# Kernel optimization log

Measured on AMD Instinct MI355X. Metric: run time of the kernel, lower is better.

## Reference

```python
import jax, jax.numpy as jnp
import numpy as np

EPS = 0.01        # TopK_custom default epsilon
MAX_ITER = 200    # TopK_custom default max_iter
GAMMA_DISC = 0.99 # RMAB discount factor (python float in original forward)
BUDGET = 40       # RMABSolver budget == soft top-k k


def setup_inputs() -> dict:
    key = jax.random.key(0)
    k1, k2 = jax.random.split(key)
    B, N = 128, 2048
    T = jax.random.uniform(k1, (B, N, 2, 2, 2), dtype=jnp.float32) + 1e-3
    T = T / T.sum(-1, keepdims=True)  # valid transition probabilities
    state = jax.random.randint(k2, (B, N), 0, 2)
    return {"T": T, "state": state}


def _whittle_indices(T, g):
    # T: [B, N, 2, 2, 2] (start_state, action, end_state); returns [B, N, 2]
    ones = jnp.ones_like(T[..., 0, 0, 0])
    zeros = jnp.zeros_like(ones)
    r1 = jnp.stack([ones,  g * T[..., 0, 0, 0] - 1, g * T[..., 0, 0, 1]], -1)
    r2 = jnp.stack([zeros, g * T[..., 0, 1, 0] - 1, g * T[..., 0, 1, 1]], -1)
    r3 = jnp.stack([ones,  g * T[..., 1, 0, 0],     g * T[..., 1, 0, 1] - 1], -1)
    r4 = jnp.stack([zeros, g * T[..., 1, 1, 0],     g * T[..., 1, 1, 1] - 1], -1)
    A1_s0 = jnp.stack([r1, r2, r3], -2)
    A2_s0 = jnp.stack([r1, r2, r4], -2)
    A1_s1 = jnp.stack([r3, r4, r1], -2)
    A2_s1 = jnp.stack([r3, r4, r2], -2)
    b_s0 = jnp.array([0.0, 0.0, -1.0], dtype=T.dtype)
    b_s1 = jnp.array([-1.0, -1.0, 0.0], dtype=T.dtype)

    def solve(A, b):
        bb = jnp.broadcast_to(b, A.shape[:-1])[..., None]
        return jnp.linalg.solve(A, bb)[..., 0]

    c1_s0 = solve(A1_s0, b_s0)
    c2_s0 = solve(A2_s0, b_s0)
    c1_s1 = solve(A1_s1, b_s1)
    c2_s1 = solve(A2_s1, b_s1)

    m_s0 = (c1_s0[..., 0] + 1.0 + g * (T[..., 1, 0, 0] * c1_s0[..., 1] + T[..., 1, 0, 1] * c1_s0[..., 2])
            >= 1.0 + g * (T[..., 1, 1, 0] * c1_s0[..., 1] + T[..., 1, 1, 1] * c1_s0[..., 2]))
    m_s1 = (c1_s1[..., 0] + g * (T[..., 0, 0, 0] * c1_s1[..., 1] + T[..., 0, 0, 1] * c1_s1[..., 2])
            >= g * (T[..., 0, 1, 0] * c1_s1[..., 1] + T[..., 0, 1, 1] * c1_s1[..., 2]))
    w0 = jnp.where(m_s0, c1_s0[..., 0], c2_s0[..., 0])
    w1 = jnp.where(m_s1, c1_s1[..., 0], c2_s1[..., 0])
    return jnp.stack([w0, w1], -1)


def _soft_topk(scores, k, eps, n_iter):
    # scores: [B, N]; Sinkhorn soft top-k (Xie et al. 2020). Returns Gamma [B, N, 2].
    n = scores.shape[-1]
    s = scores[..., None]                              # [B, N, 1]
    anchors = jnp.array([0.0, 1.0], dtype=scores.dtype)
    C_raw = (s - anchors) ** 2                         # [B, N, 2]
    C = C_raw / jnp.max(C_raw, axis=(-2, -1), keepdims=True)
    eps_log_mu = eps * jnp.log(jnp.asarray(1.0 / n, dtype=scores.dtype))
    nu = jnp.array([k / n, (n - k) / n], dtype=scores.dtype)[None, :]  # [1, 2]
    eps_log_nu = eps * jnp.log(nu)
    f0 = jnp.zeros(C.shape[:-1] + (1,), C.dtype)       # [B, N, 1]
    g0 = jnp.zeros(C.shape[:-2] + (1, 2), C.dtype)     # [B, 1, 2]

    @jax.checkpoint
    def step(carry, _):
        f, g = carry
        f = -eps * jax.nn.logsumexp(-(C - g) / eps, axis=-1, keepdims=True) + eps_log_mu
        g = -eps * jax.nn.logsumexp(-(C - f) / eps, axis=-2, keepdims=True) + eps_log_nu
        return (f, g), None

    (f, g), _ = jax.lax.scan(step, (f0, g0), None, length=n_iter)
    return jnp.exp((-C + f + g) / eps)


def reference(T, state):
    W = _whittle_indices(T, GAMMA_DISC)                       # [B, N, 2]
    W_state = jnp.take_along_axis(W, state[..., None], axis=-1)[..., 0]  # [B, N]
    Gamma = _soft_topk(-W_state, BUDGET, EPS, MAX_ITER)       # [B, N, 2]
    return Gamma[..., 0] * W_state.shape[-1]                  # act: [B, N]
```

## Files before the change

kernel.cpp:

```cpp
#include <hip/hip_runtime.h>

#define N_ARMS   2048
#define NTHREADS 256
#define EPB      8
#define N_ITER   200
#define KBUDGET  40.0f

template <int CTRL>
__device__ __forceinline__ float dpp_mov0(float x) {
    return __int_as_float(__builtin_amdgcn_update_dpp(0, __float_as_int(x), CTRL, 0xf, 0xf, true));
}
__device__ __forceinline__ float wave_sum64(float x) {
    x += dpp_mov0<0x111>(x);
    x += dpp_mov0<0x112>(x);
    x += dpp_mov0<0x114>(x);
    x += dpp_mov0<0x118>(x);
    x += dpp_mov0<0x142>(x);
    x += dpp_mov0<0x143>(x);
    return __int_as_float(__builtin_amdgcn_readlane(__float_as_int(x), 63));
}
__device__ __forceinline__ float wave_max64(float x) {
    x = fmaxf(x, dpp_mov0<0x111>(x));
    x = fmaxf(x, dpp_mov0<0x112>(x));
    x = fmaxf(x, dpp_mov0<0x114>(x));
    x = fmaxf(x, dpp_mov0<0x118>(x));
    x = fmaxf(x, dpp_mov0<0x142>(x));
    x = fmaxf(x, dpp_mov0<0x143>(x));
    return __int_as_float(__builtin_amdgcn_readlane(__float_as_int(x), 63));
}

__device__ __forceinline__ void solve3(
    float a00, float a01, float a02,
    float a10, float a11, float a12,
    float a20, float a21, float a22,
    float b0, float b1, float b2,
    float& x0, float& x1, float& x2)
{
    float M00 = a11 * a22 - a12 * a21;
    float M01 = a10 * a22 - a12 * a20;
    float M02 = a10 * a21 - a11 * a20;
    float det = a00 * M00 - a01 * M01 + a02 * M02;
    float inv = 1.0f / det;
    float N0  = b1 * a22 - a12 * b2;
    float N1  = b1 * a21 - a11 * b2;
    float N2  = a10 * b2 - b1 * a20;
    x0 = (b0 * M00 - a01 * N0 + a02 * N1) * inv;
    x1 = (a00 * N0 - b0 * M01 + a02 * N2) * inv;
    x2 = (a00 * (a11 * b2 - b1 * a21) - a01 * N2 + b0 * M02) * inv;
}

__global__ __launch_bounds__(NTHREADS, 1) void rmab_kernel(
    const float* __restrict__ T, const int* __restrict__ state,
    float* __restrict__ out)
{
    const int b    = blockIdx.x;
    const int tid  = threadIdx.x;
    const int lane = tid & 63;
    const int wid  = tid >> 6;
    const float gd = 0.99f;
    const float K_T = 100.0f * 1.4426950408889634f;

    const float* Tb  = T + (size_t)b * N_ARMS * 8;
    const int*   stb = state + (size_t)b * N_ARMS;

    float c0r[EPB], c1r[EPB];
    float mt[EPB];
    float sig[EPB];
    float cmax_local = 0.0f;

    #pragma unroll
    for (int e = 0; e < EPB; ++e) {
        int i = e * NTHREADS + tid;
        const float4* p = (const float4*)(Tb + (size_t)i * 8);
        float4 T0 = p[0];
        float4 T1 = p[1];
        int st = stb[i];
        bool s1 = (st != 0);

        float r1y = gd * T0.x - 1.0f, r1z = gd * T0.y;
        float r2y = gd * T0.z - 1.0f, r2z = gd * T0.w;
        float r3y = gd * T1.x,        r3z = gd * T1.y - 1.0f;
        float r4y = gd * T1.z,        r4z = gd * T1.w - 1.0f;

        float a01 = s1 ? r3y : r1y, a02 = s1 ? r3z : r1z;
        float a11 = s1 ? r4y : r2y, a12 = s1 ? r4z : r2z;
        float c21 = s1 ? r1y : r3y, c22 = s1 ? r1z : r3z;
        float d21 = s1 ? r2y : r4y, d22 = s1 ? r2z : r4z;
        float bv0 = s1 ? -1.0f : 0.0f;
        float bv1 = s1 ? -1.0f : 0.0f;
        float bv2 = s1 ?  0.0f : -1.0f;

        float x0, x1, x2;
        solve3(1.0f, a01, a02,  0.0f, a11, a12,  1.0f, c21, c22,
               bv0, bv1, bv2, x0, x1, x2);
        float y0, y1u, y2u;
        solve3(1.0f, a01, a02,  0.0f, a11, a12,  0.0f, d21, d22,
               bv0, bv1, bv2, y0, y1u, y2u);

        float p0 = s1 ? T0.x : T1.x;
        float p1 = s1 ? T0.y : T1.y;
        float q0 = s1 ? T0.z : T1.z;
        float q1 = s1 ? T0.w : T1.w;
        float base = s1 ? 0.0f : 1.0f;
        float lhs = x0 + base + gd * (p0 * x1 + p1 * x2);
        float rhs = base + gd * (q0 * x1 + q1 * x2);
        float w  = (lhs >= rhs) ? x0 : y0;

        float sc = -w;
        float c0 = sc * sc;
        float c1 = (sc - 1.0f) * (sc - 1.0f);
        c0r[e] = c0; c1r[e] = c1;
        cmax_local = fmaxf(cmax_local, fmaxf(c0, c1));
    }

    __shared__ __align__(16) float redS[2][4];
    __shared__ __align__(16) float redD[2][4];
    float wm = wave_max64(cmax_local);
    if (lane == 63) redS[0][wid] = wm;
    __syncthreads();
    float Cm = fmaxf(fmaxf(redS[0][0], redS[0][1]), fmaxf(redS[0][2], redS[0][3]));
    __syncthreads();

    float invCm = K_T / Cm;
    #pragma unroll
    for (int e = 0; e < EPB; ++e) {
        mt[e] = (c0r[e] - c1r[e]) * invCm;
    }

    const float DU_C = -5.6496276f;
    const float LN2  = 0.6931472f;
    float u2 = 0.0f;
    float S  = 0.0f;
    float lo = -3.4e38f, hi = 3.4e38f;
    for (int it = 0; it < N_ITER; ++it) {
        float a0 = 0.0f, a1 = 0.0f;
        float d0 = 0.0f, d1 = 0.0f;
        #pragma unroll
        for (int e = 0; e < EPB; e += 2) {
            float ex0 = __builtin_amdgcn_exp2f(mt[e]     - u2);
            float ex1 = __builtin_amdgcn_exp2f(mt[e + 1] - u2);
            float s0 = __builtin_amdgcn_rcpf(1.0f + ex0);
            float s1v = __builtin_amdgcn_rcpf(1.0f + ex1);
            sig[e] = s0; sig[e + 1] = s1v;
            a0 += s0;  a1 += s1v;
            d0 = __builtin_fmaf(-s0, s0, d0 + s0);
            d1 = __builtin_fmaf(-s1v, s1v, d1 + s1v);
        }
        float wS = wave_sum64(a0 + a1);
        float wD = wave_sum64(d0 + d1);
        int buf = it & 1;
        if (lane == 63) { redS[buf][wid] = wS; redD[buf][wid] = wD; }
        __syncthreads();
        float4 pS = *(const float4*)redS[buf];
        float4 pD = *(const float4*)redD[buf];
        S = (pS.x + pS.y) + (pS.z + pS.w);
        if (it == N_ITER - 1) break;
        float D = (pD.x + pD.y) + (pD.z + pD.w);

        float ue = u2;
        if (S < KBUDGET) lo = fmaxf(lo, ue); else hi = fminf(hi, ue);

        float Sc = fminf(fmaxf(S, 1e-4f), 2047.9f);
        float duP = (__log2f(2048.0f - Sc) - __log2f(Sc)) + DU_C;
        float duN = (KBUDGET - S) * __builtin_amdgcn_rcpf(LN2 * D);
        float cand = u2 + duN;
        bool ok = (D > 1e-20f) && (cand > lo) && (cand < hi);
        float du = ok ? duN : duP;
        u2 += du;
        if (__builtin_fabsf(du) < 1e-5f) break;
    }

    float scale = KBUDGET / S;
    float* ob = out + (size_t)b * N_ARMS;
    #pragma unroll
    for (int e = 0; e < EPB; ++e) {
        ob[e * NTHREADS + tid] = scale * sig[e];
    }
}

extern "C" void kernel_launch(void* const* d_in, const int* in_sizes, int n_in,
                              void* d_out, int out_size, void* d_ws, size_t ws_size,
                              hipStream_t stream) {
    const float* T     = (const float*)d_in[0];
    const int*   state = (const int*)d_in[1];
    float*       out   = (float*)d_out;
    int B = in_sizes[1] / N_ARMS;
    rmab_kernel<<<dim3(B), dim3(NTHREADS), 0, stream>>>(T, state, out);
}
```

Measured before the change: 64.79 us.

## Double threads per block and specialize 3x3 solves by elimination

Each batch row is now handled by 512 threads with 4 arms each instead of 256 threads with 8, so more waves run the per-iteration Newton/sigmoid loop on each CU. The generic 3x3 Cramer solve is replaced with a 2x2 solve after eliminating the known first column, which cuts setup arithmetic. The cross-wave reductions now read 8 partials, and the extra waves make each iteration's barrier more expensive.

```diff
diff --git a/kernel.cpp b/kernel.cpp
--- a/kernel.cpp
+++ b/kernel.cpp
@@ -1,8 +1,9 @@
 #include <hip/hip_runtime.h>
 
 #define N_ARMS   2048
-#define NTHREADS 256
-#define EPB      8
+#define NTHREADS 512
+#define NWAVES   (NTHREADS / 64)
+#define EPB      4
 #define N_ITER   200
 #define KBUDGET  40.0f
 
@@ -27,26 +28,6 @@
     x = fmaxf(x, dpp_mov0<0x142>(x));
     x = fmaxf(x, dpp_mov0<0x143>(x));
     return __int_as_float(__builtin_amdgcn_readlane(__float_as_int(x), 63));
-}
-
-__device__ __forceinline__ void solve3(
-    float a00, float a01, float a02,
-    float a10, float a11, float a12,
-    float a20, float a21, float a22,
-    float b0, float b1, float b2,
-    float& x0, float& x1, float& x2)
-{
-    float M00 = a11 * a22 - a12 * a21;
-    float M01 = a10 * a22 - a12 * a20;
-    float M02 = a10 * a21 - a11 * a20;
-    float det = a00 * M00 - a01 * M01 + a02 * M02;
-    float inv = 1.0f / det;
-    float N0  = b1 * a22 - a12 * b2;
-    float N1  = b1 * a21 - a11 * b2;
-    float N2  = a10 * b2 - b1 * a20;
-    x0 = (b0 * M00 - a01 * N0 + a02 * N1) * inv;
-    x1 = (a00 * N0 - b0 * M01 + a02 * N2) * inv;
-    x2 = (a00 * (a11 * b2 - b1 * a21) - a01 * N2 + b0 * M02) * inv;
 }
 
 __global__ __launch_bounds__(NTHREADS, 1) void rmab_kernel(
@@ -86,16 +67,21 @@
         float a11 = s1 ? r4y : r2y, a12 = s1 ? r4z : r2z;
         float c21 = s1 ? r1y : r3y, c22 = s1 ? r1z : r3z;
         float d21 = s1 ? r2y : r4y, d22 = s1 ? r2z : r4z;
-        float bv0 = s1 ? -1.0f : 0.0f;
-        float bv1 = s1 ? -1.0f : 0.0f;
-        float bv2 = s1 ?  0.0f : -1.0f;
+        float bv01 = s1 ? -1.0f : 0.0f;
+        float bv2  = s1 ?  0.0f : -1.0f;
 
-        float x0, x1, x2;
-        solve3(1.0f, a01, a02,  0.0f, a11, a12,  1.0f, c21, c22,
-               bv0, bv1, bv2, x0, x1, x2);
-        float y0, y1u, y2u;
-        solve3(1.0f, a01, a02,  0.0f, a11, a12,  0.0f, d21, d22,
-               bv0, bv1, bv2, y0, y1u, y2u);
+        float e21 = c21 - a01, e22 = c22 - a02, r2 = bv2 - bv01;
+        float det1 = a11 * e22 - a12 * e21;
+        float inv1 = 1.0f / det1;
+        float x1 = (bv01 * e22 - a12 * r2) * inv1;
+        float x2 = (a11 * r2 - bv01 * e21) * inv1;
+        float x0 = bv01 - a01 * x1 - a02 * x2;
+
+        float det2 = a11 * d22 - a12 * d21;
+        float inv2 = 1.0f / det2;
+        float y1 = (bv01 * d22 - a12 * bv2) * inv2;
+        float y2 = (a11 * bv2 - bv01 * d21) * inv2;
+        float y0 = bv01 - a01 * y1 - a02 * y2;
 
         float p0 = s1 ? T0.x : T1.x;
         float p1 = s1 ? T0.y : T1.y;
@@ -113,12 +99,14 @@
         cmax_local = fmaxf(cmax_local, fmaxf(c0, c1));
     }
 
-    __shared__ __align__(16) float redS[2][4];
-    __shared__ __align__(16) float redD[2][4];
+    __shared__ __align__(16) float redS[2][NWAVES];
+    __shared__ __align__(16) float redD[2][NWAVES];
     float wm = wave_max64(cmax_local);
     if (lane == 63) redS[0][wid] = wm;
     __syncthreads();
-    float Cm = fmaxf(fmaxf(redS[0][0], redS[0][1]), fmaxf(redS[0][2], redS[0][3]));
+    float Cm = redS[0][0];
+    #pragma unroll
+    for (int wv = 1; wv < NWAVES; ++wv) Cm = fmaxf(Cm, redS[0][wv]);
     __syncthreads();
 
     float invCm = K_T / Cm;
@@ -151,14 +139,13 @@
         int buf = it & 1;
         if (lane == 63) { redS[buf][wid] = wS; redD[buf][wid] = wD; }
         __syncthreads();
-        float4 pS = *(const float4*)redS[buf];
-        float4 pD = *(const float4*)redD[buf];
-        S = (pS.x + pS.y) + (pS.z + pS.w);
+        S = redS[buf][0];
+        float D = redD[buf][0];
+        #pragma unroll
+        for (int wv = 1; wv < NWAVES; ++wv) { S += redS[buf][wv]; D += redD[buf][wv]; }
         if (it == N_ITER - 1) break;
-        float D = (pD.x + pD.y) + (pD.z + pD.w);
 
-        float ue = u2;
-        if (S < KBUDGET) lo = fmaxf(lo, ue); else hi = fminf(hi, ue);
+        if (S < KBUDGET) lo = fmaxf(lo, u2); else hi = fminf(hi, u2);
 
         float Sc = fminf(fmaxf(S, 1e-4f), 2047.9f);
         float duP = (__log2f(2048.0f - Sc) - __log2f(Sc)) + DU_C;
```

New measurement: 64.31 us. Within noise of the previous version (-0.7%).
